# Kernel optimization log

Measured on AMD Instinct MI355X. Metric: run time of the kernel, lower is better.

## Reference

```python
import jax, jax.numpy as jnp
import numpy as np

N = 10000
E = 160000
H = 8
C = 128
D = 1024
NB = 3
NG = 64
NEG_SLOPE = 0.2
BN_EPS = 1e-5


def setup_inputs() -> dict:
    key = jax.random.key(0)
    ks = jax.random.split(key, 12)
    x = jax.random.normal(ks[0], (N, D), dtype=jnp.float32)
    edge_index = jax.random.randint(ks[1], (2, E), 0, N, dtype=jnp.int64)
    batch = jnp.sort(jax.random.randint(ks[2], (N,), 0, NG, dtype=jnp.int64))
    W = jax.random.normal(ks[3], (NB, D, D), dtype=jnp.float32) * 0.03
    att_src = jax.random.normal(ks[4], (NB, H, C), dtype=jnp.float32) * 0.1
    att_dst = jax.random.normal(ks[5], (NB, H, C), dtype=jnp.float32) * 0.1
    att_bias = jnp.zeros((NB, D), dtype=jnp.float32)
    gamma = jnp.ones((NB, D), dtype=jnp.float32)
    beta = jnp.zeros((NB, D), dtype=jnp.float32)
    W_out = jax.random.normal(ks[6], (D, 2), dtype=jnp.float32) * 0.03
    b_out = jnp.zeros((2,), dtype=jnp.float32)
    return {"x": x, "edge_index": edge_index, "batch": batch, "W": W,
            "att_src": att_src, "att_dst": att_dst, "att_bias": att_bias,
            "gamma": gamma, "beta": beta, "W_out": W_out, "b_out": b_out}


def _gat_conv(x, Wb, a_src, a_dst, bias, src, dst):
    # linear projection, per-head view: [N, H, C]
    h = (x @ Wb).reshape(N, H, C)
    alpha_src = jnp.einsum('nhc,hc->nh', h, a_src)  # [N,H]
    alpha_dst = jnp.einsum('nhc,hc->nh', h, a_dst)
    e = jax.nn.leaky_relu(alpha_src[src] + alpha_dst[dst], NEG_SLOPE)  # [Etot,H]
    # segment softmax over incoming edges per destination node
    m = jax.ops.segment_max(e, dst, num_segments=N)  # every node has self-loop
    ex = jnp.exp(e - m[dst])
    denom = jax.ops.segment_sum(ex, dst, num_segments=N)
    alpha = ex / denom[dst]  # [Etot,H]
    msg = alpha[:, :, None] * h[src]  # [Etot,H,C]
    out = jax.ops.segment_sum(msg, dst, num_segments=N).reshape(N, H * C)
    return out + bias


def _batchnorm(x, g, b):
    mu = jnp.mean(x, axis=0)
    var = jnp.mean(jnp.square(x - mu), axis=0)  # biased, training mode
    return (x - mu) * jax.lax.rsqrt(var + BN_EPS) * g + b


def reference(x, edge_index, batch, W, att_src, att_dst, att_bias, gamma, beta, W_out, b_out):
    # add self loops (PyG GATConv default)
    loop = jnp.arange(N, dtype=edge_index.dtype)
    src = jnp.concatenate([edge_index[0], loop])
    dst = jnp.concatenate([edge_index[1], loop])

    h = x
    prev = x
    for i in range(NB):
        att = _gat_conv(h, W[i], att_src[i], att_dst[i], att_bias[i], src, dst)
        o = jax.nn.relu(_batchnorm(prev + att, gamma[i], beta[i]))
        prev = h
        h = o

    # global mean pool over graphs
    sums = jax.ops.segment_sum(h, batch, num_segments=NG)
    cnts = jax.ops.segment_sum(jnp.ones((N,), dtype=h.dtype), batch, num_segments=NG)
    pooled = sums / jnp.maximum(cnts, 1.0)[:, None]
    return pooled @ W_out + b_out
```

## Files before the change

### kernel.cpp

```cpp
#include <hip/hip_runtime.h>
#include <hip/hip_bf16.h>

#define N_NODES 10000
#define E_EDGES 160000
#define ETOT    170000
#define H_HEADS 8
#define C_CH    128
#define D_DIM   1024
#define NBLK    3
#define NGRAPH  64
#define NEG_SLOPE 0.2f
#define BN_EPS  1e-5f

typedef __attribute__((ext_vector_type(8))) _Float16 half8;
typedef __attribute__((ext_vector_type(4))) _Float16 half4;
typedef __attribute__((ext_vector_type(2))) _Float16 half2v;
typedef __attribute__((ext_vector_type(4))) float f32x4;

__device__ inline int lower_bound_batch(const int* __restrict__ batch, int g) {
    int lo = 0, hi = N_NODES;
    while (lo < hi) {
        int mid = (lo + hi) >> 1;
        if (batch[mid] < g) lo = mid + 1;
        else hi = mid;
    }
    return lo;
}

__global__ void deg_kernel(const int* __restrict__ ei, int* __restrict__ deg) {
    int tid = blockIdx.x * blockDim.x + threadIdx.x;
    if (tid >= ETOT) return;
    int dst = (tid < E_EDGES) ? ei[E_EDGES + tid] : (tid - E_EDGES);
    atomicAdd(&deg[dst], 1);
}

__global__ void scan_kernel(const int* __restrict__ deg, int* __restrict__ ioff) {
    __shared__ int part[256];
    int t = threadIdx.x;
    const int CH = (N_NODES + 255) / 256;
    int base = t * CH;
    int s = 0;
    for (int j = 0; j < CH; ++j) {
        int idx = base + j;
        if (idx < N_NODES) s += deg[idx];
    }
    part[t] = s;
    __syncthreads();
    for (int o = 1; o < 256; o <<= 1) {
        int v = 0;
        if (t >= o) v = part[t - o];
        __syncthreads();
        part[t] += v;
        __syncthreads();
    }
    int run = (t == 0) ? 0 : part[t - 1];
    for (int j = 0; j < CH; ++j) {
        int idx = base + j;
        if (idx < N_NODES) { ioff[idx] = run; run += deg[idx]; }
    }
}

__global__ void scatter_kernel(const int* __restrict__ ei, int* __restrict__ ioff,
                               int* __restrict__ csr_src, int* __restrict__ csr_dst) {
    int tid = blockIdx.x * blockDim.x + threadIdx.x;
    if (tid >= ETOT) return;
    int src, dst;
    if (tid < E_EDGES) { src = ei[tid]; dst = ei[E_EDGES + tid]; }
    else { src = dst = tid - E_EDGES; }
    int pos = atomicAdd(&ioff[dst], 1);
    csr_src[pos] = src;
    csr_dst[pos] = dst;
}

__global__ __launch_bounds__(256) void xconv_kernel(const float* __restrict__ in,
                                                    _Float16* __restrict__ o, int n4) {
    int i = blockIdx.x * blockDim.x + threadIdx.x;
    if (i >= n4) return;
    float4 v = ((const float4*)in)[i];
    half4 h = {(_Float16)v.x, (_Float16)v.y, (_Float16)v.z, (_Float16)v.w};
    ((half4*)o)[i] = h;
}

__global__ __launch_bounds__(256) void wtconv_kernel(const float* __restrict__ Wall,
                                                     _Float16* __restrict__ t16all) {
    const float* W = Wall + (size_t)blockIdx.z * D_DIM * D_DIM;
    _Float16* t16 = t16all + (size_t)blockIdx.z * D_DIM * D_DIM;
    __shared__ float t[32][33];
    int bn = blockIdx.x * 32;
    int bk = blockIdx.y * 32;
    int tx = threadIdx.x & 31;
    int ty = threadIdx.x >> 5;
#pragma unroll
    for (int r = 0; r < 32; r += 8)
        t[ty + r][tx] = W[(size_t)(bk + ty + r) * D_DIM + bn + tx];
    __syncthreads();
#pragma unroll
    for (int r = 0; r < 32; r += 8)
        t16[(size_t)(bn + ty + r) * D_DIM + bk + tx] = (_Float16)t[tx][ty + r];
}

__global__ __launch_bounds__(256) void gemm_mfma_kernel(const _Float16* __restrict__ A,
                                                        const _Float16* __restrict__ Bt,
                                                        _Float16* __restrict__ Hout,
                                                        const float* __restrict__ att_s,
                                                        const float* __restrict__ att_d,
                                                        float* __restrict__ asrc,
                                                        float* __restrict__ adst,
                                                        float* __restrict__ stats, int M) {
    __shared__ short As[128 * 64];
    __shared__ short Bs[128 * 64];
    __shared__ float sA[128], sD[128];
    int bx = blockIdx.x;
    int tid = threadIdx.x;
    if (bx == 0) {
#pragma unroll
        for (int j = 0; j < 8; ++j) stats[tid + j * 256] = 0.f;
    }
    int c = bx & 7;
    int head = (bx >> 3) & 7;
    int mt = c + 8 * (bx >> 6);
    if (mt >= 79) return;
    int bm = mt * 128;
    int bn = head * 128;
    int wave = tid >> 6;
    int lane = tid & 63;
    int wm = (wave >> 1) * 64;
    int wn = (wave & 1) * 64;
    int quad = lane >> 4;
    int l16 = lane & 15;

    f32x4 acc[4][4];
#pragma unroll
    for (int i = 0; i < 4; ++i)
#pragma unroll
        for (int j = 0; j < 4; ++j) acc[i][j] = (f32x4){0.f, 0.f, 0.f, 0.f};

    int srow8 = lane >> 3;
    int sswz = ((lane & 7) ^ srow8) << 4;
    const char* gA[4];
    const char* gB[4];
    char* ldA[4];
    char* ldB[4];
#pragma unroll
    for (int r = 0; r < 4; ++r) {
        int arow = wave * 8 + r * 32 + srow8;
        int ga = bm + arow;
        if (ga > M - 1) ga = M - 1;
        gA[r] = (const char*)(A + (size_t)ga * 1024) + sswz;
        gB[r] = (const char*)(Bt + (size_t)(bn + arow) * 1024) + sswz;
        ldA[r] = (char*)As + (wave * 8 + r * 32) * 128;
        ldB[r] = (char*)Bs + (wave * 8 + r * 32) * 128;
    }

    int xr = l16 & 7;
    for (int kb = 0; kb < 16; ++kb) {
        int ko = kb * 128;
#pragma unroll
        for (int r = 0; r < 4; ++r) {
            __builtin_amdgcn_global_load_lds(
                (const __attribute__((address_space(1))) void*)(gA[r] + ko),
                (__attribute__((address_space(3))) void*)ldA[r], 16, 0, 0);
            __builtin_amdgcn_global_load_lds(
                (const __attribute__((address_space(1))) void*)(gB[r] + ko),
                (__attribute__((address_space(3))) void*)ldB[r], 16, 0, 0);
        }
        __syncthreads();
#pragma unroll
        for (int h = 0; h < 2; ++h) {
            int sl = (quad + h * 4) ^ xr;
            half8 af[4], bfr[4];
#pragma unroll
            for (int i = 0; i < 4; ++i)
                af[i] = *(const half8*)(As + (wm + i * 16 + l16) * 64 + sl * 8);
#pragma unroll
            for (int j = 0; j < 4; ++j)
                bfr[j] = *(const half8*)(Bs + (wn + j * 16 + l16) * 64 + sl * 8);
#pragma unroll
            for (int i = 0; i < 4; ++i)
#pragma unroll
                for (int j = 0; j < 4; ++j)
                    acc[i][j] = __builtin_amdgcn_mfma_f32_16x16x32_f16(af[i], bfr[j], acc[i][j], 0, 0, 0);
        }
        __syncthreads();
    }

    float wsv[4], wdv[4];
#pragma unroll
    for (int j = 0; j < 4; ++j) {
        int cc = wn + j * 16 + l16;
        wsv[j] = att_s[head * 128 + cc];
        wdv[j] = att_d[head * 128 + cc];
    }
    float psv[4][4], pdv[4][4];
#pragma unroll
    for (int i = 0; i < 4; ++i) {
#pragma unroll
        for (int reg = 0; reg < 4; ++reg) {
            float p = acc[i][0][reg] * wsv[0] + acc[i][1][reg] * wsv[1] +
                      acc[i][2][reg] * wsv[2] + acc[i][3][reg] * wsv[3];
            float q = acc[i][0][reg] * wdv[0] + acc[i][1][reg] * wdv[1] +
                      acc[i][2][reg] * wdv[2] + acc[i][3][reg] * wdv[3];
#pragma unroll
            for (int o = 1; o < 16; o <<= 1) {
                p += __shfl_xor(p, o);
                q += __shfl_xor(q, o);
            }
            psv[i][reg] = p;
            pdv[i][reg] = q;
        }
    }
    if ((wave & 1) == 0 && l16 == 0) {
#pragma unroll
        for (int i = 0; i < 4; ++i)
#pragma unroll
            for (int reg = 0; reg < 4; ++reg) {
                int r = wm + i * 16 + quad * 4 + reg;
                sA[r] = psv[i][reg];
                sD[r] = pdv[i][reg];
            }
    }
#pragma unroll
    for (int i = 0; i < 4; ++i) {
#pragma unroll
        for (int reg = 0; reg < 4; ++reg) {
            int gr = bm + wm + i * 16 + quad * 4 + reg;
            if (gr < M) {
                _Float16* hp = Hout + (size_t)head * N_NODES * 128 + (size_t)gr * 128 + wn + l16;
#pragma unroll
                for (int j = 0; j < 4; ++j) hp[j * 16] = (_Float16)acc[i][j][reg];
            }
        }
    }
    __syncthreads();
    if ((wave & 1) == 1 && l16 == 0) {
#pragma unroll
        for (int i = 0; i < 4; ++i)
#pragma unroll
            for (int reg = 0; reg < 4; ++reg) {
                int r = wm + i * 16 + quad * 4 + reg;
                int gr = bm + r;
                if (gr < M) {
                    asrc[gr * 8 + head] = sA[r] + psv[i][reg];
                    adst[gr * 8 + head] = sD[r] + pdv[i][reg];
                }
            }
    }
}

__global__ __launch_bounds__(256) void edge_exp_kernel(const int* __restrict__ csr_src,
                                                       const int* __restrict__ csr_dst,
                                                       const float* __restrict__ asrc,
                                                       const float* __restrict__ adst,
                                                       float* __restrict__ exw) {
    int p = blockIdx.x * 256 + threadIdx.x;
    if (p >= ETOT) return;
    int s = csr_src[p];
    int d = csr_dst[p];
    float4 s0 = *(const float4*)(asrc + (unsigned)s * 8u);
    float4 s1 = *(const float4*)(asrc + (unsigned)s * 8u + 4u);
    float4 d0 = *(const float4*)(adst + (unsigned)d * 8u);
    float4 d1 = *(const float4*)(adst + (unsigned)d * 8u + 4u);
    float e[8] = {s0.x + d0.x, s0.y + d0.y, s0.z + d0.z, s0.w + d0.w,
                  s1.x + d1.x, s1.y + d1.y, s1.z + d1.z, s1.w + d1.w};
    float4 o0, o1;
#pragma unroll
    for (int j = 0; j < 8; ++j) {
        float v = e[j];
        v = (v > 0.f) ? v : NEG_SLOPE * v;
        float ex = __expf(v);
        if (j < 4) ((float*)&o0)[j] = ex;
        else ((float*)&o1)[j - 4] = ex;
    }
    *(float4*)(exw + (unsigned)p * 8u) = o0;
    *(float4*)(exw + (unsigned)p * 8u + 4u) = o1;
}

__global__ __launch_bounds__(256) void agg_kernel(const _Float16* __restrict__ h16,
                                                  const float* __restrict__ exw,
                                                  const int* __restrict__ ioff,
                                                  const int* __restrict__ csr_src,
                                                  const _Float16* __restrict__ prevh,
                                                  const float* __restrict__ bias,
                                                  _Float16* __restrict__ yout) {
    int bx = blockIdx.x;
    int tid = threadIdx.x;
    int head = bx & 7;
    int chunk = bx >> 3;
    int sub = tid >> 5;
    int lane = tid & 31;
    int n = chunk * 8 + sub;
    unsigned c4 = (unsigned)(lane * 4);
    const _Float16* hh = h16 + (size_t)head * N_NODES * 128;
    const float* exh = exw + head;
    int start = (n == 0) ? 0 : ioff[n - 1];
    int end = ioff[n];
    float den = 0.f;
    float4 acc = make_float4(0.f, 0.f, 0.f, 0.f);
    int p = start;
    for (; p + 4 <= end; p += 4) {
        int s0 = csr_src[p + 0];
        int s1 = csr_src[p + 1];
        int s2 = csr_src[p + 2];
        int s3 = csr_src[p + 3];
        float x0 = exh[(unsigned)p * 8u];
        float x1 = exh[(unsigned)p * 8u + 8u];
        float x2 = exh[(unsigned)p * 8u + 16u];
        float x3 = exh[(unsigned)p * 8u + 24u];
        half4 h0 = *(const half4*)(hh + ((unsigned)s0 * 128u + c4));
        half4 h1 = *(const half4*)(hh + ((unsigned)s1 * 128u + c4));
        half4 h2 = *(const half4*)(hh + ((unsigned)s2 * 128u + c4));
        half4 h3 = *(const half4*)(hh + ((unsigned)s3 * 128u + c4));
        den += (x0 + x1) + (x2 + x3);
        acc.x = fmaf(x0, (float)h0[0], fmaf(x1, (float)h1[0], fmaf(x2, (float)h2[0], fmaf(x3, (float)h3[0], acc.x))));
        acc.y = fmaf(x0, (float)h0[1], fmaf(x1, (float)h1[1], fmaf(x2, (float)h2[1], fmaf(x3, (float)h3[1], acc.y))));
        acc.z = fmaf(x0, (float)h0[2], fmaf(x1, (float)h1[2], fmaf(x2, (float)h2[2], fmaf(x3, (float)h3[2], acc.z))));
        acc.w = fmaf(x0, (float)h0[3], fmaf(x1, (float)h1[3], fmaf(x2, (float)h2[3], fmaf(x3, (float)h3[3], acc.w))));
    }
    for (; p < end; ++p) {
        int s = csr_src[p];
        float x = exh[(unsigned)p * 8u];
        half4 hv = *(const half4*)(hh + ((unsigned)s * 128u + c4));
        den += x;
        acc.x = fmaf(x, (float)hv[0], acc.x);
        acc.y = fmaf(x, (float)hv[1], acc.y);
        acc.z = fmaf(x, (float)hv[2], acc.z);
        acc.w = fmaf(x, (float)hv[3], acc.w);
    }
    float invd = 1.0f / den;
    int col = head * 128 + (int)c4;
    half4 ph = *(const half4*)(prevh + (size_t)n * 1024 + col);
    float4 bv = *(const float4*)(bias + col);
    float r0 = fmaf(acc.x, invd, (float)ph[0] + bv.x);
    float r1 = fmaf(acc.y, invd, (float)ph[1] + bv.y);
    float r2 = fmaf(acc.z, invd, (float)ph[2] + bv.z);
    float r3 = fmaf(acc.w, invd, (float)ph[3] + bv.w);
    half4 o = {(_Float16)r0, (_Float16)r1, (_Float16)r2, (_Float16)r3};
    *(half4*)(yout + (size_t)n * 1024 + col) = o;
}

__global__ void bn_stats_kernel(const _Float16* __restrict__ y, float* __restrict__ stats) {
    int col = (blockIdx.x * 256 + threadIdx.x) * 2;
    float s0 = 0.f, s1 = 0.f, q0 = 0.f, q1 = 0.f;
    for (int r = blockIdx.y; r < N_NODES; r += gridDim.y) {
        half2v v = *(const half2v*)(y + (size_t)r * 1024 + col);
        float a = (float)v[0], b = (float)v[1];
        s0 += a; q0 += a * a;
        s1 += b; q1 += b * b;
    }
    atomicAdd(&stats[col], s0);
    atomicAdd(&stats[col + 1], s1);
    atomicAdd(&stats[1024 + col], q0);
    atomicAdd(&stats[1024 + col + 1], q1);
}

__global__ void bn_apply_kernel(const _Float16* __restrict__ y, const float* __restrict__ stats,
                                const float* __restrict__ gamma, const float* __restrict__ beta,
                                _Float16* __restrict__ oout) {
    int idx4 = blockIdx.x * blockDim.x + threadIdx.x;
    if (idx4 >= N_NODES * D_DIM / 4) return;
    int base = idx4 * 4;
    int col = base & 1023;
    const float invN = 1.0f / (float)N_NODES;
    half4 v = ((const half4*)y)[idx4];
    float r[4];
#pragma unroll
    for (int j = 0; j < 4; ++j) {
        int cc = col + j;
        float mu = stats[cc] * invN;
        float var = stats[1024 + cc] * invN - mu * mu;
        float t = ((float)v[j] - mu) * rsqrtf(var + BN_EPS) * gamma[cc] + beta[cc];
        r[j] = fmaxf(t, 0.f);
    }
    half4 h = {(_Float16)r[0], (_Float16)r[1], (_Float16)r[2], (_Float16)r[3]};
    ((half4*)oout)[idx4] = h;
}

__global__ __launch_bounds__(256) void pool_kernel(const _Float16* __restrict__ h3,
                                                   const int* __restrict__ batch,
                                                   float* __restrict__ pooled) {
    int g = blockIdx.y;
    int col = threadIdx.x * 4;
    int lo = lower_bound_batch(batch, g);
    int hi = lower_bound_batch(batch, g + 1);
    int len = hi - lo;
    int r0 = lo + (int)(((long long)len * blockIdx.x) >> 3);
    int r1 = lo + (int)(((long long)len * (blockIdx.x + 1)) >> 3);
    float a0 = 0.f, a1 = 0.f, a2 = 0.f, a3 = 0.f;
    for (int r = r0; r < r1; ++r) {
        half4 v = *(const half4*)(h3 + (size_t)r * 1024 + col);
        a0 += (float)v[0]; a1 += (float)v[1]; a2 += (float)v[2]; a3 += (float)v[3];
    }
    if (r1 > r0) {
        atomicAdd(&pooled[(size_t)g * 1024 + col + 0], a0);
        atomicAdd(&pooled[(size_t)g * 1024 + col + 1], a1);
        atomicAdd(&pooled[(size_t)g * 1024 + col + 2], a2);
        atomicAdd(&pooled[(size_t)g * 1024 + col + 3], a3);
    }
}

__global__ void final_kernel(const float* __restrict__ pooled, const int* __restrict__ batch,
                             const float* __restrict__ Wout, const float* __restrict__ bout,
                             float* __restrict__ out) {
    int g = blockIdx.x;
    int t = threadIdx.x;
    float p0 = 0.f, p1 = 0.f;
    for (int d = t; d < 1024; d += 256) {
        float v = pooled[(size_t)g * 1024 + d];
        p0 = fmaf(v, Wout[2 * d], p0);
        p1 = fmaf(v, Wout[2 * d + 1], p1);
    }
    __shared__ float s0[256], s1[256];
    s0[t] = p0; s1[t] = p1;
    __syncthreads();
    for (int o = 128; o; o >>= 1) {
        if (t < o) { s0[t] += s0[t + o]; s1[t] += s1[t + o]; }
        __syncthreads();
    }
    if (t == 0) {
        int cnt = lower_bound_batch(batch, g + 1) - lower_bound_batch(batch, g);
        float inv = 1.0f / fmaxf((float)cnt, 1.0f);
        out[g * 2 + 0] = s0[0] * inv + bout[0];
        out[g * 2 + 1] = s1[0] * inv + bout[1];
    }
}

extern "C" void kernel_launch(void* const* d_in, const int* in_sizes, int n_in,
                              void* d_out, int out_size, void* d_ws, size_t ws_size,
                              hipStream_t stream) {
    const float* x        = (const float*)d_in[0];
    const int*   ei       = (const int*)d_in[1];
    const int*   batch    = (const int*)d_in[2];
    const float* W        = (const float*)d_in[3];
    const float* att_src  = (const float*)d_in[4];
    const float* att_dst  = (const float*)d_in[5];
    const float* att_bias = (const float*)d_in[6];
    const float* gamma    = (const float*)d_in[7];
    const float* beta     = (const float*)d_in[8];
    const float* Wout     = (const float*)d_in[9];
    const float* bout     = (const float*)d_in[10];
    float* out = (float*)d_out;

    const size_t ND = (size_t)N_NODES * D_DIM;
    float* ws = (float*)d_ws;
    float* asrc   = ws;
    float* adst   = asrc + (size_t)N_NODES * H_HEADS;
    float* stats  = adst + (size_t)N_NODES * H_HEADS;
    float* pooled = stats + 2 * D_DIM;
    int* ideg     = (int*)(pooled + (size_t)NGRAPH * D_DIM);
    int* ioff     = ideg + N_NODES;
    int* csr_src  = ioff + N_NODES;
    int* csr_dst  = csr_src + ETOT;
    float* exw    = (float*)(csr_dst + ETOT);
    _Float16* bufP  = (_Float16*)(exw + (size_t)ETOT * H_HEADS);
    _Float16* bufO0 = bufP + ND;
    _Float16* h16   = bufO0 + ND;
    _Float16* y16   = h16 + ND;
    _Float16* Wt3   = y16 + ND;

    hipMemsetAsync(ideg, 0, N_NODES * sizeof(int), stream);
    hipMemsetAsync(pooled, 0, (size_t)NGRAPH * D_DIM * sizeof(float), stream);
    deg_kernel<<<(ETOT + 255) / 256, 256, 0, stream>>>(ei, ideg);
    scan_kernel<<<1, 256, 0, stream>>>(ideg, ioff);
    scatter_kernel<<<(ETOT + 255) / 256, 256, 0, stream>>>(ei, ioff, csr_src, csr_dst);
    xconv_kernel<<<(int)(ND / 4 + 255) / 256, 256, 0, stream>>>(x, bufP, (int)(ND / 4));
    wtconv_kernel<<<dim3(32, 32, 3), 256, 0, stream>>>(W, Wt3);

    const _Float16* Ain[3]  = {bufP, bufO0, bufP};
    const _Float16* Pin[3]  = {bufP, bufP, bufO0};
    _Float16* Oout[3]       = {bufO0, bufP, bufP};

    for (int i = 0; i < NBLK; ++i) {
        gemm_mfma_kernel<<<640, 256, 0, stream>>>(
            Ain[i], Wt3 + (size_t)i * D_DIM * D_DIM, h16,
            att_src + i * H_HEADS * C_CH, att_dst + i * H_HEADS * C_CH,
            asrc, adst, stats, N_NODES);
        edge_exp_kernel<<<(ETOT + 255) / 256, 256, 0, stream>>>(csr_src, csr_dst,
                                                                asrc, adst, exw);
        agg_kernel<<<N_NODES, 256, 0, stream>>>(h16, exw, ioff, csr_src,
                                                Pin[i], att_bias + i * D_DIM, y16);
        bn_stats_kernel<<<dim3(2, 128), 256, 0, stream>>>(y16, stats);
        bn_apply_kernel<<<(int)(ND / 4 + 255) / 256, 256, 0, stream>>>(
            y16, stats, gamma + i * D_DIM, beta + i * D_DIM, Oout[i]);
    }

    pool_kernel<<<dim3(8, NGRAPH), 256, 0, stream>>>(bufP, batch, pooled);
    final_kernel<<<NGRAPH, 256, 0, stream>>>(pooled, batch, Wout, bout, out);
}
```

Baseline: 578.0 us.

## Halve GEMM N-tile to 64 columns and reduce attention logits via atomics

```diff
diff --git a/kernel.cpp b/kernel.cpp
--- a/kernel.cpp
+++ b/kernel.cpp
@@ -99,17 +99,16 @@
         t16[(size_t)(bn + ty + r) * D_DIM + bk + tx] = (_Float16)t[tx][ty + r];
 }
 
-__global__ __launch_bounds__(256) void gemm_mfma_kernel(const _Float16* __restrict__ A,
-                                                        const _Float16* __restrict__ Bt,
-                                                        _Float16* __restrict__ Hout,
-                                                        const float* __restrict__ att_s,
-                                                        const float* __restrict__ att_d,
-                                                        float* __restrict__ asrc,
-                                                        float* __restrict__ adst,
-                                                        float* __restrict__ stats, int M) {
+__global__ __launch_bounds__(256, 4) void gemm_mfma_kernel(const _Float16* __restrict__ A,
+                                                           const _Float16* __restrict__ Bt,
+                                                           _Float16* __restrict__ Hout,
+                                                           const float* __restrict__ att_s,
+                                                           const float* __restrict__ att_d,
+                                                           float* __restrict__ asrc,
+                                                           float* __restrict__ adst,
+                                                           float* __restrict__ stats, int M) {
     __shared__ short As[128 * 64];
-    __shared__ short Bs[128 * 64];
-    __shared__ float sA[128], sD[128];
+    __shared__ short Bs[64 * 64];
     int bx = blockIdx.x;
     int tid = threadIdx.x;
     if (bx == 0) {
@@ -117,38 +116,43 @@
         for (int j = 0; j < 8; ++j) stats[tid + j * 256] = 0.f;
     }
     int c = bx & 7;
-    int head = (bx >> 3) & 7;
-    int mt = c + 8 * (bx >> 6);
+    int nt = (bx >> 3) & 15;
+    int mt = c + 8 * (bx >> 7);
     if (mt >= 79) return;
     int bm = mt * 128;
-    int bn = head * 128;
+    int head = nt >> 1;
+    int bncol = (nt & 1) * 64;
+    int bnrow = nt * 64;
     int wave = tid >> 6;
     int lane = tid & 63;
-    int wm = (wave >> 1) * 64;
-    int wn = (wave & 1) * 64;
+    int wm = wave * 32;
     int quad = lane >> 4;
     int l16 = lane & 15;
 
-    f32x4 acc[4][4];
-#pragma unroll
-    for (int i = 0; i < 4; ++i)
+    f32x4 acc[2][4];
+#pragma unroll
+    for (int i = 0; i < 2; ++i)
 #pragma unroll
         for (int j = 0; j < 4; ++j) acc[i][j] = (f32x4){0.f, 0.f, 0.f, 0.f};
 
     int srow8 = lane >> 3;
     int sswz = ((lane & 7) ^ srow8) << 4;
     const char* gA[4];
-    const char* gB[4];
+    const char* gB[2];
     char* ldA[4];
-    char* ldB[4];
+    char* ldB[2];
 #pragma unroll
     for (int r = 0; r < 4; ++r) {
         int arow = wave * 8 + r * 32 + srow8;
         int ga = bm + arow;
         if (ga > M - 1) ga = M - 1;
         gA[r] = (const char*)(A + (size_t)ga * 1024) + sswz;
-        gB[r] = (const char*)(Bt + (size_t)(bn + arow) * 1024) + sswz;
         ldA[r] = (char*)As + (wave * 8 + r * 32) * 128;
+    }
+#pragma unroll
+    for (int r = 0; r < 2; ++r) {
+        int brow = wave * 8 + r * 32 + srow8;
+        gB[r] = (const char*)(Bt + (size_t)(bnrow + brow) * 1024) + sswz;
         ldB[r] = (char*)Bs + (wave * 8 + r * 32) * 128;
     }
 
@@ -156,27 +160,28 @@
     for (int kb = 0; kb < 16; ++kb) {
         int ko = kb * 128;
 #pragma unroll
-        for (int r = 0; r < 4; ++r) {
+        for (int r = 0; r < 4; ++r)
             __builtin_amdgcn_global_load_lds(
                 (const __attribute__((address_space(1))) void*)(gA[r] + ko),
                 (__attribute__((address_space(3))) void*)ldA[r], 16, 0, 0);
+#pragma unroll
+        for (int r = 0; r < 2; ++r)
             __builtin_amdgcn_global_load_lds(
                 (const __attribute__((address_space(1))) void*)(gB[r] + ko),
                 (__attribute__((address_space(3))) void*)ldB[r], 16, 0, 0);
-        }
         __syncthreads();
 #pragma unroll
         for (int h = 0; h < 2; ++h) {
             int sl = (quad + h * 4) ^ xr;
-            half8 af[4], bfr[4];
-#pragma unroll
-            for (int i = 0; i < 4; ++i)
+            half8 af[2], bfr[4];
+#pragma unroll
+            for (int i = 0; i < 2; ++i)
                 af[i] = *(const half8*)(As + (wm + i * 16 + l16) * 64 + sl * 8);
 #pragma unroll
             for (int j = 0; j < 4; ++j)
-                bfr[j] = *(const half8*)(Bs + (wn + j * 16 + l16) * 64 + sl * 8);
-#pragma unroll
-            for (int i = 0; i < 4; ++i)
+                bfr[j] = *(const half8*)(Bs + (j * 16 + l16) * 64 + sl * 8);
+#pragma unroll
+            for (int i = 0; i < 2; ++i)
 #pragma unroll
                 for (int j = 0; j < 4; ++j)
                     acc[i][j] = __builtin_amdgcn_mfma_f32_16x16x32_f16(af[i], bfr[j], acc[i][j], 0, 0, 0);
@@ -187,13 +192,12 @@
     float wsv[4], wdv[4];
 #pragma unroll
     for (int j = 0; j < 4; ++j) {
-        int cc = wn + j * 16 + l16;
+        int cc = bncol + j * 16 + l16;
         wsv[j] = att_s[head * 128 + cc];
         wdv[j] = att_d[head * 128 + cc];
     }
-    float psv[4][4], pdv[4][4];
-#pragma unroll
-    for (int i = 0; i < 4; ++i) {
+#pragma unroll
+    for (int i = 0; i < 2; ++i) {
 #pragma unroll
         for (int reg = 0; reg < 4; ++reg) {
             float p = acc[i][0][reg] * wsv[0] + acc[i][1][reg] * wsv[1] +
@@ -205,45 +209,26 @@
                 p += __shfl_xor(p, o);
                 q += __shfl_xor(q, o);
             }
-            psv[i][reg] = p;
-            pdv[i][reg] = q;
+            if (l16 == 0) {
+                int gr = bm + wm + i * 16 + quad * 4 + reg;
+                if (gr < M) {
+                    atomicAdd(&asrc[gr * 8 + head], p);
+                    atomicAdd(&adst[gr * 8 + head], q);
+                }
+            }
         }
     }
-    if ((wave & 1) == 0 && l16 == 0) {
-#pragma unroll
-        for (int i = 0; i < 4; ++i)
-#pragma unroll
-            for (int reg = 0; reg < 4; ++reg) {
-                int r = wm + i * 16 + quad * 4 + reg;
-                sA[r] = psv[i][reg];
-                sD[r] = pdv[i][reg];
-            }
-    }
-#pragma unroll
-    for (int i = 0; i < 4; ++i) {
+#pragma unroll
+    for (int i = 0; i < 2; ++i) {
 #pragma unroll
         for (int reg = 0; reg < 4; ++reg) {
             int gr = bm + wm + i * 16 + quad * 4 + reg;
             if (gr < M) {
-                _Float16* hp = Hout + (size_t)head * N_NODES * 128 + (size_t)gr * 128 + wn + l16;
+                _Float16* hp = Hout + (size_t)head * N_NODES * 128 + (size_t)gr * 128 + bncol + l16;
 #pragma unroll
                 for (int j = 0; j < 4; ++j) hp[j * 16] = (_Float16)acc[i][j][reg];
             }
         }
-    }
-    __syncthreads();
-    if ((wave & 1) == 1 && l16 == 0) {
-#pragma unroll
-        for (int i = 0; i < 4; ++i)
-#pragma unroll
-            for (int reg = 0; reg < 4; ++reg) {
-                int r = wm + i * 16 + quad * 4 + reg;
-                int gr = bm + r;
-                if (gr < M) {
-                    asrc[gr * 8 + head] = sA[r] + psv[i][reg];
-                    adst[gr * 8 + head] = sD[r] + pdv[i][reg];
-                }
-            }
     }
 }
 
@@ -355,8 +340,10 @@
 
 __global__ void bn_apply_kernel(const _Float16* __restrict__ y, const float* __restrict__ stats,
                                 const float* __restrict__ gamma, const float* __restrict__ beta,
-                                _Float16* __restrict__ oout) {
+                                _Float16* __restrict__ oout, float* __restrict__ azero) {
     int idx4 = blockIdx.x * blockDim.x + threadIdx.x;
+    if (idx4 < 2 * N_NODES * H_HEADS / 4)
+        ((float4*)azero)[idx4] = make_float4(0.f, 0.f, 0.f, 0.f);
     if (idx4 >= N_NODES * D_DIM / 4) return;
     int base = idx4 * 4;
     int col = base & 1023;
@@ -459,6 +446,7 @@
 
     hipMemsetAsync(ideg, 0, N_NODES * sizeof(int), stream);
     hipMemsetAsync(pooled, 0, (size_t)NGRAPH * D_DIM * sizeof(float), stream);
+    hipMemsetAsync(asrc, 0, (size_t)2 * N_NODES * H_HEADS * sizeof(float), stream);
     deg_kernel<<<(ETOT + 255) / 256, 256, 0, stream>>>(ei, ideg);
     scan_kernel<<<1, 256, 0, stream>>>(ideg, ioff);
     scatter_kernel<<<(ETOT + 255) / 256, 256, 0, stream>>>(ei, ioff, csr_src, csr_dst);
@@ -470,7 +458,7 @@
     _Float16* Oout[3]       = {bufO0, bufP, bufP};
 
     for (int i = 0; i < NBLK; ++i) {
-        gemm_mfma_kernel<<<640, 256, 0, stream>>>(
+        gemm_mfma_kernel<<<1280, 256, 0, stream>>>(
             Ain[i], Wt3 + (size_t)i * D_DIM * D_DIM, h16,
             att_src + i * H_HEADS * C_CH, att_dst + i * H_HEADS * C_CH,
             asrc, adst, stats, N_NODES);
@@ -480,7 +468,7 @@
                                                 Pin[i], att_bias + i * D_DIM, y16);
         bn_stats_kernel<<<dim3(2, 128), 256, 0, stream>>>(y16, stats);
         bn_apply_kernel<<<(int)(ND / 4 + 255) / 256, 256, 0, stream>>>(
-            y16, stats, gamma + i * D_DIM, beta + i * D_DIM, Oout[i]);
+            y16, stats, gamma + i * D_DIM, beta + i * D_DIM, Oout[i], asrc);
     }
 
     pool_kernel<<<dim3(8, NGRAPH), 256, 0, stream>>>(bufP, batch, pooled);
```

New measurement: 572.6 us. About the same (-0.9%).
